# Performance work log

Hardware: AMD Instinct MI355X
Metric: run time of the kernel (lower is better)

Reference implementation:

```python
import jax, jax.numpy as jnp
import numpy as np

C = 768
H = 12
HD = C // H
SCALE = HD ** -0.5
EPS = 1e-5


def setup_inputs() -> dict:
    key = jax.random.key(0)
    kit = iter(jax.random.split(key, 40))
    r = lambda *s: jax.random.normal(next(kit), s, jnp.float32) * 0.02
    d = dict(
        s_x=jax.random.normal(next(kit), (8, 196, C), jnp.float32),
        t_x=jax.random.normal(next(kit), (8, 1568, C), jnp.float32),
        ln1s_g=jnp.ones(C), ln1s_b=jnp.zeros(C),
        mha_w=r(3 * C, C), mha_b=r(3 * C), mha_ow=r(C, C), mha_ob=r(C),
        ln1t_g=jnp.ones(C), ln1t_b=jnp.zeros(C),
        attn_qkv_w=r(3 * C, C), attn_q_b=r(C), attn_v_b=r(C), attn_pw=r(C, C), attn_pb=r(C),
        lnt2s_g=jnp.ones(C), lnt2s_b=jnp.zeros(C),
        t2s_qw=r(C, C), t2s_qb=r(C), t2s_kvw=r(2 * C, C), t2s_kvb=r(C), t2s_pw=r(C, C), t2s_pb=r(C),
        lns2t_g=jnp.ones(C), lns2t_b=jnp.zeros(C),
        s2t_qw=r(C, C), s2t_qb=r(C), s2t_kvw=r(2 * C, C), s2t_kvb=r(C), s2t_pw=r(C, C), s2t_pb=r(C),
        ln2s_g=jnp.ones(C), ln2s_b=jnp.zeros(C),
        cfc_w=r(4 * C, C), cfc_b=r(4 * C), cproj_w=r(C, 4 * C), cproj_b=r(C),
        ln2t_g=jnp.ones(C), ln2t_b=jnp.zeros(C),
        fc1_w=r(4 * C, C), fc1_b=r(4 * C), fc2_w=r(C, 4 * C), fc2_b=r(C),
    )
    return d


def ln(x, g, b):
    m = x.mean(-1, keepdims=True)
    v = jnp.mean((x - m) ** 2, -1, keepdims=True)
    return (x - m) * jax.lax.rsqrt(v + EPS) * g + b


def heads(x):  # (B, N, C) -> (B, H, N, HD)
    B, N, _ = x.shape
    return x.reshape(B, N, H, HD).transpose(0, 2, 1, 3)


def mhsa(q, k, v):  # (B, H, Nq, HD), (B, H, Nk, HD) -> (B, Nq, C)
    a = jax.nn.softmax(jnp.einsum('bhqd,bhkd->bhqk', q * SCALE, k), axis=-1)
    o = jnp.einsum('bhqk,bhkd->bhqd', a, v)
    B, _, Nq, _ = o.shape
    return o.transpose(0, 2, 1, 3).reshape(B, Nq, C)


def reference(s_x, t_x, ln1s_g, ln1s_b, mha_w, mha_b, mha_ow, mha_ob,
              ln1t_g, ln1t_b, attn_qkv_w, attn_q_b, attn_v_b, attn_pw, attn_pb,
              lnt2s_g, lnt2s_b, t2s_qw, t2s_qb, t2s_kvw, t2s_kvb, t2s_pw, t2s_pb,
              lns2t_g, lns2t_b, s2t_qw, s2t_qb, s2t_kvw, s2t_kvb, s2t_pw, s2t_pb,
              ln2s_g, ln2s_b, cfc_w, cfc_b, cproj_w, cproj_b,
              ln2t_g, ln2t_b, fc1_w, fc1_b, fc2_w, fc2_b):
    # 1) clip self-attention. torch nn.MultiheadAttention (batch_first=False)
    # treats axis 0 of the (B, s_N, C) input as the sequence dim, so we
    # faithfully attend over the batch axis.
    y = ln(s_x, ln1s_g, ln1s_b)
    qkv = y @ mha_w.T + mha_b  # (B, s_N, 3C)
    q, k, v = jnp.split(qkv, 3, axis=-1)
    qt, kt, vt = (a.transpose(1, 0, 2) for a in (q, k, v))  # (s_N, B, C)
    o = mhsa(heads(qt), heads(kt), heads(vt))  # (s_N, B, C)
    o = o @ mha_ow.T + mha_ob
    s_x = s_x + o.transpose(1, 0, 2)

    # 2) video-stream self-attention (qkv_bias=True -> cat(q_b, 0, v_b))
    y = ln(t_x, ln1t_g, ln1t_b)
    qkv_bias = jnp.concatenate([attn_q_b, jnp.zeros_like(attn_v_b), attn_v_b])
    qkv = y @ attn_qkv_w.T + qkv_bias
    q, k, v = jnp.split(qkv, 3, axis=-1)
    o = mhsa(heads(q), heads(k), heads(v))
    t_x = t_x + (o @ attn_pw.T + attn_pb)

    # 3) T2S cross: query from LN(s_x), key/value from (updated, un-normed) t_x
    ys = ln(s_x, lnt2s_g, lnt2s_b)
    q = ys @ t2s_qw.T + t2s_qb
    kv = t_x @ t2s_kvw.T + jnp.concatenate([jnp.zeros_like(t2s_kvb), t2s_kvb])
    k, v = jnp.split(kv, 2, axis=-1)
    o = mhsa(heads(q), heads(k), heads(v))
    s_x = s_x + (o @ t2s_pw.T + t2s_pb)

    # 4) S2T cross: query from LN(t_x), key/value from updated s_x
    yt = ln(t_x, lns2t_g, lns2t_b)
    q = yt @ s2t_qw.T + s2t_qb
    kv = s_x @ s2t_kvw.T + jnp.concatenate([jnp.zeros_like(s2t_kvb), s2t_kvb])
    k, v = jnp.split(kv, 2, axis=-1)
    o = mhsa(heads(q), heads(k), heads(v))
    t_x = t_x + (o @ s2t_pw.T + s2t_pb)

    # 5) clip MLP (QuickGELU)
    y = ln(s_x, ln2s_g, ln2s_b)
    h = y @ cfc_w.T + cfc_b
    h = h * jax.nn.sigmoid(1.702 * h)
    s_x = s_x + (h @ cproj_w.T + cproj_b)

    # 6) video MLP (exact GELU, torch default)
    y = ln(t_x, ln2t_g, ln2t_b)
    h = jax.nn.gelu(y @ fc1_w.T + fc1_b, approximate=False)
    t_x = t_x + (h @ fc2_w.T + fc2_b)
    return (s_x, t_x)
```

## Files before the change

kernel.cpp:

```cpp
#include <hip/hip_runtime.h>
#include <stdint.h>


typedef uint16_t u16;
typedef uint16_t u16x8 __attribute__((ext_vector_type(8)));
typedef uint16_t u16x4 __attribute__((ext_vector_type(4)));
typedef short bf16x8 __attribute__((ext_vector_type(8)));
typedef float f32x4 __attribute__((ext_vector_type(4)));

__device__ __forceinline__ float b2f(u16 u) {
    union { float f; uint32_t i; } x;
    x.i = ((uint32_t)u) << 16;
    return x.f;
}
__device__ __forceinline__ u16 f2b(float f) {
    union { float f; uint32_t i; } x;
    x.f = f;
    uint32_t i = x.i;
    uint32_t r = (i + 0x7FFFu + ((i >> 16) & 1u)) >> 16;
    return (u16)r;
}
__device__ __forceinline__ u16 f2b_trunc(float f) {
    union { float f; uint32_t i; } x;
    x.f = f;
    return (u16)(x.i >> 16);
}

__device__ __forceinline__ void gload16(const u16* g, u16* l) {
    __builtin_amdgcn_global_load_lds(
        (const __attribute__((address_space(1))) uint32_t*)g,
        (__attribute__((address_space(3))) uint32_t*)l, 16, 0, 0);
}

__global__ void f2b_kernel(const float* __restrict__ in, u16* __restrict__ out, int n) {
    int i = blockIdx.x * 256 + threadIdx.x;
    if (i < n) out[i] = f2b(in[i]);
}
__global__ void copy_f32(const float* __restrict__ in, float* __restrict__ out, int n) {
    int i = blockIdx.x * 256 + threadIdx.x;
    if (i < n) out[i] = in[i];
}

__global__ void build_bias_pool(float* __restrict__ dst,
    const float* mha_b, const float* attn_q_b, const float* attn_v_b,
    const float* mha_ob, const float* attn_pb, const float* t2s_kvb,
    const float* t2s_qb, const float* t2s_pb, const float* s2t_qb,
    const float* s2t_kvb, const float* s2t_pb, const float* cfc_b,
    const float* cproj_b, const float* fc1_b, const float* fc2_b) {
    int i = blockIdx.x * 256 + threadIdx.x;
    float v = 0.f;
    if (i < 2304) v = mha_b[i];
    else if (i < 4608) { int j = i - 2304; v = (j < 768) ? attn_q_b[j] : (j < 1536 ? 0.f : attn_v_b[j - 1536]); }
    else if (i < 5376) v = mha_ob[i - 4608];
    else if (i < 6144) v = attn_pb[i - 5376];
    else if (i < 7680) { int j = i - 6144; v = (j < 768) ? 0.f : t2s_kvb[j - 768]; }
    else if (i < 8448) v = t2s_qb[i - 7680];
    else if (i < 9216) v = t2s_pb[i - 8448];
    else if (i < 9984) v = s2t_qb[i - 9216];
    else if (i < 11520) { int j = i - 9984; v = (j < 768) ? 0.f : s2t_kvb[j - 768]; }
    else if (i < 12288) v = s2t_pb[i - 11520];
    else if (i < 15360) v = cfc_b[i - 12288];
    else if (i < 16128) v = cproj_b[i - 15360];
    else if (i < 19200) v = fc1_b[i - 16128];
    else if (i < 19968) v = fc2_b[i - 19200];
    else return;
    dst[i] = v;
}

__device__ __forceinline__ float block_sum(float v, float* red) {
    #pragma unroll
    for (int o = 32; o > 0; o >>= 1) v += __shfl_down(v, o, 64);
    int w = threadIdx.x >> 6, l = threadIdx.x & 63;
    __syncthreads();
    if (l == 0) red[w] = v;
    __syncthreads();
    return red[0] + red[1] + red[2] + red[3];
}

__global__ __launch_bounds__(256) void ln_kernel(
    const float* __restrict__ x, const float* __restrict__ g,
    const float* __restrict__ bta, u16* __restrict__ y) {
    const int r = blockIdx.x;
    const int t = threadIdx.x;
    const float* xr = x + (size_t)r * 768;
    float v0 = xr[t], v1 = xr[t + 256], v2 = xr[t + 512];
    __shared__ float red[4];
    float mean = block_sum(v0 + v1 + v2, red) * (1.0f / 768.0f);
    float d0 = v0 - mean, d1 = v1 - mean, d2 = v2 - mean;
    float var = block_sum(d0 * d0 + d1 * d1 + d2 * d2, red) * (1.0f / 768.0f);
    float rs = rsqrtf(var + 1e-5f);
    u16* yr = y + (size_t)r * 768;
    yr[t]       = f2b(d0 * rs * g[t]       + bta[t]);
    yr[t + 256] = f2b(d1 * rs * g[t + 256] + bta[t + 256]);
    yr[t + 512] = f2b(d2 * rs * g[t + 512] + bta[t + 512]);
}

__global__ __launch_bounds__(256) void transpose_v(
    const u16* __restrict__ vp, u16* __restrict__ vt, int Nk, int Nkp,
    long long vA, long long vJ) {
    const int inst = blockIdx.y;
    const int a = inst / 12, h = inst % 12;
    const int t0 = blockIdx.x * 64;
    const int tid = threadIdx.x;
    __shared__ u16 T[64][72];
    const int kvl = tid >> 2, dseg = (tid & 3) * 16;
    u16x8 v0 = {}, v1 = {};
    if (t0 + kvl < Nk) {
        const u16* src = vp + a * vA + (long long)(t0 + kvl) * vJ + h * 64 + dseg;
        v0 = *(const u16x8*)src;
        v1 = *(const u16x8*)(src + 8);
    }
    *(u16x8*)&T[kvl][dseg]     = v0;
    *(u16x8*)&T[kvl][dseg + 8] = v1;
    __syncthreads();
    const int dl = tid >> 2, kseg = (tid & 3) * 16;
    u16x8 w0, w1;
    #pragma unroll
    for (int j = 0; j < 8; j++) w0[j] = T[kseg + j][dl];
    #pragma unroll
    for (int j = 0; j < 8; j++) w1[j] = T[kseg + 8 + j][dl];
    u16* orow = vt + ((size_t)inst * 64 + dl) * Nkp + t0 + kseg;
    *(u16x8*)orow = w0;
    *(u16x8*)(orow + 8) = w1;
}

template <int MODE, int BM>
__global__ __launch_bounds__(256) void gemm_mfma(
    const u16* __restrict__ A, const u16* __restrict__ W,
    const float* __restrict__ bias, u16* __restrict__ Cb,
    float* __restrict__ Cf, int M, int N, int K) {
    constexpr int MI = BM / 32;
    __shared__ u16 As[2][BM][32];
    __shared__ u16 Bs[2][128][32];
    const int tid = threadIdx.x;
    const int lane = tid & 63;
    const int wid = tid >> 6;
    const int wr = (wid >> 1) * (BM / 2), wc = (wid & 1) * 64;
    const int m0 = blockIdx.x * BM, n0 = blockIdx.y * 128;
    const int lr = lane >> 2, lc = (lane & 3) * 8;
    const int fr = lane & 15, fk = (lane >> 4) * 8;
    const int abase = wid * (BM / 4);
    const int bbase = wid * 32;
    f32x4 acc[MI][4] = {};
    for (int k0 = 0; k0 < K; k0 += 64) {
        #pragma unroll
        for (int s = 0; s < 2; s++) {
            #pragma unroll
            for (int j = 0; j < BM / 64; j++) {
                int rowa = m0 + abase + j * 16 + lr;
                rowa = rowa < M ? rowa : M - 1;
                gload16(A + (size_t)rowa * K + k0 + s * 32 + lc, &As[s][abase + j * 16][0]);
            }
            #pragma unroll
            for (int j = 0; j < 2; j++) {
                gload16(W + (size_t)(n0 + bbase + j * 16 + lr) * K + k0 + s * 32 + lc,
                        &Bs[s][bbase + j * 16][0]);
            }
        }
        __syncthreads();
        #pragma unroll
        for (int s = 0; s < 2; s++) {
            bf16x8 a[MI], b[4];
            #pragma unroll
            for (int i = 0; i < MI; i++) a[i] = *(const bf16x8*)&As[s][wr + i * 16 + fr][fk];
            #pragma unroll
            for (int j = 0; j < 4; j++) b[j] = *(const bf16x8*)&Bs[s][wc + j * 16 + fr][fk];
            #pragma unroll
            for (int i = 0; i < MI; i++)
                #pragma unroll
                for (int j = 0; j < 4; j++)
                    acc[i][j] = __builtin_amdgcn_mfma_f32_16x16x32_bf16(a[i], b[j], acc[i][j], 0, 0, 0);
        }
        __syncthreads();
    }
    const int er = (lane >> 4) * 4;
    #pragma unroll
    for (int i = 0; i < MI; i++) {
        #pragma unroll
        for (int reg = 0; reg < 4; reg++) {
            int r = m0 + wr + i * 16 + er + reg;
            if (r >= M) continue;
            #pragma unroll
            for (int j = 0; j < 4; j++) {
                int c = n0 + wc + j * 16 + fr;
                float v = acc[i][j][reg] + bias[c];
                size_t idx = (size_t)r * N + c;
                if (MODE == 1) {
                    Cf[idx] += v;
                } else if (MODE == 4) {
                    float nv = Cf[idx] + v;
                    Cf[idx] = nv;
                    Cb[idx] = f2b(nv);
                } else {
                    if (MODE == 2) v = v / (1.0f + expf(-1.702f * v));
                    if (MODE == 3) v = 0.5f * v * (1.0f + erff(v * 0.70710678118654752f));
                    Cb[idx] = f2b(v);
                }
            }
        }
    }
}

__global__ __launch_bounds__(256) void flash_attn(
    const u16* __restrict__ qp, const u16* __restrict__ kp,
    const u16* __restrict__ vt, u16* __restrict__ op,
    int Nq, int Nk, int Nkp,
    long long qA, long long qI, long long kA, long long kJ,
    long long oA, long long oI) {
    const int inst = blockIdx.y;
    const int a = inst / 12, h = inst % 12;
    const int tid = threadIdx.x, lane = tid & 63, w = tid >> 6;
    const int fr = lane & 15, g = lane >> 4, fk = g * 8;
    const int f3s = (fr & 7) << 3;
    __shared__ u16 Ks[64][64];
    __shared__ u16 Vs[64][64];
    __shared__ u16 Ps[4][16][64];
    const u16* qb = qp + a * qA + h * 64;
    const u16* kb = kp + a * kA + h * 64;
    const u16* vtb = vt + (size_t)inst * 64 * Nkp;
    const int q0 = blockIdx.x * 64 + w * 16;

    bf16x8 qf[2];
    {
        u16x8 raw0 = {}, raw1 = {};
        int qr = q0 + fr;
        if (qr < Nq) {
            const u16* qrp = qb + (long long)qr * qI;
            raw0 = *(const u16x8*)(qrp + fk);
            raw1 = *(const u16x8*)(qrp + 32 + fk);
        }
        const float QS = 0.125f * 1.44269504088896340736f;
        u16x8 s0, s1;
        #pragma unroll
        for (int e = 0; e < 8; e++) {
            s0[e] = f2b(b2f(raw0[e]) * QS);
            s1[e] = f2b(b2f(raw1[e]) * QS);
        }
        qf[0] = *(bf16x8*)&s0;
        qf[1] = *(bf16x8*)&s1;
    }
    float mrun = -1e30f, lrun = 0.f;
    f32x4 o[4] = {};

    const int l = lane;
    const int srow = w * 8 + (l >> 3);
    const int sdcol = ((l & 7) * 8) ^ (((l >> 3) & 7) << 3);

    for (int t0 = 0; t0 < Nk; t0 += 64) {
        #pragma unroll
        for (int c = 0; c < 2; c++) {
            int row = c * 32 + srow;
            int kr = t0 + row; if (kr >= Nk) kr = Nk - 1;
            gload16(kb + (long long)kr * kJ + sdcol, &Ks[0][0] + c * 2048 + w * 512);
            gload16(vtb + (size_t)row * Nkp + t0 + sdcol, &Vs[0][0] + c * 2048 + w * 512);
        }
        __syncthreads();

        f32x4 s[4] = {};
        #pragma unroll
        for (int hh = 0; hh < 4; hh++) {
            bf16x8 k0f = *(const bf16x8*)&Ks[hh * 16 + fr][fk ^ f3s];
            bf16x8 k1f = *(const bf16x8*)&Ks[hh * 16 + fr][(32 + fk) ^ f3s];
            s[hh] = __builtin_amdgcn_mfma_f32_16x16x32_bf16(k0f, qf[0], s[hh], 0, 0, 0);
            s[hh] = __builtin_amdgcn_mfma_f32_16x16x32_bf16(k1f, qf[1], s[hh], 0, 0, 0);
        }
        float lmax = -1e30f;
        if (t0 + 64 <= Nk) {
            #pragma unroll
            for (int hh = 0; hh < 4; hh++)
                #pragma unroll
                for (int r = 0; r < 4; r++) lmax = fmaxf(lmax, s[hh][r]);
        } else {
            #pragma unroll
            for (int hh = 0; hh < 4; hh++)
                #pragma unroll
                for (int r = 0; r < 4; r++) {
                    if (t0 + hh * 16 + 4 * g + r >= Nk) s[hh][r] = -1e30f;
                    lmax = fmaxf(lmax, s[hh][r]);
                }
        }
        lmax = fmaxf(lmax, __shfl_xor(lmax, 16, 64));
        lmax = fmaxf(lmax, __shfl_xor(lmax, 32, 64));
        if (!__all(lmax <= mrun + 8.0f)) {
            float mn = fmaxf(mrun, lmax);
            float sf = exp2f(mrun - mn);
            mrun = mn;
            lrun *= sf;
            float sfo[4];
            #pragma unroll
            for (int r = 0; r < 4; r++) sfo[r] = __shfl(sf, g * 4 + r, 64);
            #pragma unroll
            for (int dt = 0; dt < 4; dt++)
                #pragma unroll
                for (int r = 0; r < 4; r++) o[dt][r] *= sfo[r];
        }
        float p[4][4];
        float ps = 0.f;
        #pragma unroll
        for (int hh = 0; hh < 4; hh++)
            #pragma unroll
            for (int r = 0; r < 4; r++) {
                p[hh][r] = exp2f(s[hh][r] - mrun);
                ps += p[hh][r];
            }
        ps += __shfl_xor(ps, 16, 64);
        ps += __shfl_xor(ps, 32, 64);
        lrun += ps;
        #pragma unroll
        for (int hh = 0; hh < 4; hh++) {
            u16x4 pk;
            #pragma unroll
            for (int r = 0; r < 4; r++) pk[r] = f2b_trunc(p[hh][r]);
            *(u16x4*)&Ps[w][fr][(hh * 16 + g * 4) ^ f3s] = pk;
        }
        bf16x8 pa0 = *(const bf16x8*)&Ps[w][fr][fk ^ f3s];
        bf16x8 pa1 = *(const bf16x8*)&Ps[w][fr][(32 + fk) ^ f3s];
        #pragma unroll
        for (int dt = 0; dt < 4; dt++) {
            bf16x8 vf0 = *(const bf16x8*)&Vs[dt * 16 + fr][fk ^ f3s];
            bf16x8 vf1 = *(const bf16x8*)&Vs[dt * 16 + fr][(32 + fk) ^ f3s];
            o[dt] = __builtin_amdgcn_mfma_f32_16x16x32_bf16(pa0, vf0, o[dt], 0, 0, 0);
            o[dt] = __builtin_amdgcn_mfma_f32_16x16x32_bf16(pa1, vf1, o[dt], 0, 0, 0);
        }
        __syncthreads();
    }
    float rcp = 1.0f / lrun;
    #pragma unroll
    for (int r = 0; r < 4; r++) {
        float rr = __shfl(rcp, g * 4 + r, 64);
        int q = q0 + g * 4 + r;
        if (q >= Nq) continue;
        u16* orow = op + a * oA + (long long)q * oI + h * 64;
        #pragma unroll
        for (int dt = 0; dt < 4; dt++)
            orow[dt * 16 + fr] = f2b(o[dt][r] * rr);
    }
}

extern "C" void kernel_launch(void* const* d_in, const int* in_sizes, int n_in,
                              void* d_out, int out_size, void* d_ws, size_t ws_size,
                              hipStream_t stream) {
    const int B = 8, sN = 196, tN = 1568;
    const int Ms = B * sN;
    const int Mt = B * tN;
    const int n_sf = Ms * 768;
    const int n_tf = Mt * 768;
    (void)n_in; (void)out_size; (void)ws_size;

    const bool dict_order = (in_sizes[0] == n_sf);
    auto IN = [&](int di, int ai) -> const float* {
        return (const float*)d_in[dict_order ? di : ai];
    };
    const float* in_sx      = IN(0, 35);
    const float* in_tx      = IN(1, 42);
    const float* ln1s_g     = IN(2, 14);
    const float* ln1s_b     = IN(3, 13);
    const float* mha_w      = IN(4, 28);
    const float* mha_b      = IN(5, 25);
    const float* mha_ow     = IN(6, 27);
    const float* mha_ob     = IN(7, 26);
    const float* ln1t_g     = IN(8, 16);
    const float* ln1t_b     = IN(9, 15);
    const float* attn_qkv_w = IN(10, 3);
    const float* attn_q_b   = IN(11, 2);
    const float* attn_v_b   = IN(12, 4);
    const float* attn_pw    = IN(13, 1);
    const float* attn_pb    = IN(14, 0);
    const float* lnt2s_g    = IN(15, 24);
    const float* lnt2s_b    = IN(16, 23);
    const float* t2s_qw     = IN(17, 41);
    const float* t2s_qb     = IN(18, 40);
    const float* t2s_kvw    = IN(19, 37);
    const float* t2s_kvb    = IN(20, 36);
    const float* t2s_pw     = IN(21, 39);
    const float* t2s_pb     = IN(22, 38);
    const float* lns2t_g    = IN(23, 22);
    const float* lns2t_b    = IN(24, 21);
    const float* s2t_qw     = IN(25, 34);
    const float* s2t_qb     = IN(26, 33);
    const float* s2t_kvw    = IN(27, 30);
    const float* s2t_kvb    = IN(28, 29);
    const float* s2t_pw     = IN(29, 32);
    const float* s2t_pb     = IN(30, 31);
    const float* ln2s_g     = IN(31, 18);
    const float* ln2s_b     = IN(32, 17);
    const float* cfc_w      = IN(33, 6);
    const float* cfc_b      = IN(34, 5);
    const float* cproj_w    = IN(35, 8);
    const float* cproj_b    = IN(36, 7);
    const float* ln2t_g     = IN(37, 20);
    const float* ln2t_b     = IN(38, 19);
    const float* fc1_w      = IN(39, 10);
    const float* fc1_b      = IN(40, 9);
    const float* fc2_w      = IN(41, 12);
    const float* fc2_b      = IN(42, 11);

    float* s_f = (float*)d_out;
    float* t_f = (float*)d_out + n_sf;

    char* ws = (char*)d_ws;
    size_t off = 0;
    auto take = [&](size_t bytes) { size_t o = off; off += (bytes + 255) & ~(size_t)255; return o; };
    float* biasP = (float*)(ws + take(19968 * 4));
    u16*   yb    = (u16*)(ws + take((size_t)Mt * 768 * 2));
    u16*   bufA  = (u16*)(ws + take((size_t)Mt * 2304 * 2));
    u16*   bufB  = (u16*)(ws + take((size_t)Mt * 768 * 2));
    u16*   sxb   = (u16*)(ws + take((size_t)Ms * 768 * 2));
    u16*   vtb   = (u16*)(ws + take((size_t)2352 * 64 * 64 * 2));
    auto wtake = [&](size_t nelem) { return (u16*)(ws + take(nelem * 2)); };
    u16 *W_mha   = wtake(2304 * 768), *W_mhao  = wtake(768 * 768);
    u16 *W_qkv   = wtake(2304 * 768), *W_attnp = wtake(768 * 768);
    u16 *W_t2sq  = wtake(768 * 768),  *W_t2skv = wtake(1536 * 768), *W_t2sp = wtake(768 * 768);
    u16 *W_s2tq  = wtake(768 * 768),  *W_s2tkv = wtake(1536 * 768), *W_s2tp = wtake(768 * 768);
    u16 *W_cfc   = wtake(3072 * 768), *W_cproj = wtake(768 * 3072);
    u16 *W_fc1   = wtake(3072 * 768), *W_fc2   = wtake(768 * 3072);

    const int B_MHA = 0, B_QKV = 2304, B_MHAO = 4608, B_ATTNP = 5376;
    const int B_T2SKV = 6144, B_T2SQ = 7680, B_T2SP = 8448, B_S2TQ = 9216;
    const int B_S2TKV = 9984, B_S2TP = 11520, B_CFC = 12288, B_CPROJ = 15360;
    const int B_FC1 = 16128, B_FC2 = 19200;

    auto cdiv = [](int a, int b) { return (a + b - 1) / b; };
    auto CW = [&](const float* src, u16* dst, int n) {
        f2b_kernel<<<cdiv(n, 256), 256, 0, stream>>>(src, dst, n);
    };
    CW(mha_w, W_mha, 2304 * 768);      CW(mha_ow, W_mhao, 768 * 768);
    CW(attn_qkv_w, W_qkv, 2304 * 768); CW(attn_pw, W_attnp, 768 * 768);
    CW(t2s_qw, W_t2sq, 768 * 768);     CW(t2s_kvw, W_t2skv, 1536 * 768);
    CW(t2s_pw, W_t2sp, 768 * 768);     CW(s2t_qw, W_s2tq, 768 * 768);
    CW(s2t_kvw, W_s2tkv, 1536 * 768);  CW(s2t_pw, W_s2tp, 768 * 768);
    CW(cfc_w, W_cfc, 3072 * 768);      CW(cproj_w, W_cproj, 768 * 3072);
    CW(fc1_w, W_fc1, 3072 * 768);      CW(fc2_w, W_fc2, 768 * 3072);

    build_bias_pool<<<78, 256, 0, stream>>>(biasP,
        mha_b, attn_q_b, attn_v_b, mha_ob, attn_pb, t2s_kvb, t2s_qb, t2s_pb,
        s2t_qb, s2t_kvb, s2t_pb, cfc_b, cproj_b, fc1_b, fc2_b);

    copy_f32<<<cdiv(n_sf, 256), 256, 0, stream>>>(in_sx, s_f, n_sf);
    copy_f32<<<cdiv(n_tf, 256), 256, 0, stream>>>(in_tx, t_f, n_tf);

    ln_kernel<<<Ms, 256, 0, stream>>>(s_f, ln1s_g, ln1s_b, yb);
    gemm_mfma<0, 64><<<dim3(cdiv(Ms, 64), 18), 256, 0, stream>>>(yb, W_mha, biasP + B_MHA, bufA, (float*)0, Ms, 2304, 768);
    transpose_v<<<dim3(1, sN * 12), 256, 0, stream>>>(bufA + 1536, vtb, 8, 64, 2304LL, (long long)sN * 2304);
    flash_attn<<<dim3(1, sN * 12), 256, 0, stream>>>(
        bufA, bufA + 768, vtb, bufB, 8, 8, 64,
        2304LL, (long long)sN * 2304,
        2304LL, (long long)sN * 2304,
        768LL,  (long long)sN * 768);
    gemm_mfma<1, 64><<<dim3(cdiv(Ms, 64), 6), 256, 0, stream>>>(bufB, W_mhao, biasP + B_MHAO, (u16*)0, s_f, Ms, 768, 768);

    ln_kernel<<<Mt, 256, 0, stream>>>(t_f, ln1t_g, ln1t_b, yb);
    gemm_mfma<0, 128><<<dim3(cdiv(Mt, 128), 18), 256, 0, stream>>>(yb, W_qkv, biasP + B_QKV, bufA, (float*)0, Mt, 2304, 768);
    transpose_v<<<dim3(25, B * 12), 256, 0, stream>>>(bufA + 1536, vtb, tN, 1600, (long long)tN * 2304, 2304LL);
    flash_attn<<<dim3(cdiv(tN, 64), B * 12), 256, 0, stream>>>(
        bufA, bufA + 768, vtb, bufB, tN, tN, 1600,
        (long long)tN * 2304, 2304LL,
        (long long)tN * 2304, 2304LL,
        (long long)tN * 768, 768LL);
    gemm_mfma<4, 128><<<dim3(cdiv(Mt, 128), 6), 256, 0, stream>>>(bufB, W_attnp, biasP + B_ATTNP, yb, t_f, Mt, 768, 768);

    gemm_mfma<0, 128><<<dim3(cdiv(Mt, 128), 12), 256, 0, stream>>>(yb, W_t2skv, biasP + B_T2SKV, bufA, (float*)0, Mt, 1536, 768);
    transpose_v<<<dim3(25, B * 12), 256, 0, stream>>>(bufA + 768, vtb, tN, 1600, (long long)tN * 1536, 1536LL);
    ln_kernel<<<Ms, 256, 0, stream>>>(s_f, lnt2s_g, lnt2s_b, yb);
    u16* q3 = bufB;
    u16* o3 = bufB + (size_t)Ms * 768;
    gemm_mfma<0, 64><<<dim3(cdiv(Ms, 64), 6), 256, 0, stream>>>(yb, W_t2sq, biasP + B_T2SQ, q3, (float*)0, Ms, 768, 768);
    flash_attn<<<dim3(cdiv(sN, 64), B * 12), 256, 0, stream>>>(
        q3, bufA, vtb, o3, sN, tN, 1600,
        (long long)sN * 768, 768LL,
        (long long)tN * 1536, 1536LL,
        (long long)sN * 768, 768LL);
    gemm_mfma<4, 64><<<dim3(cdiv(Ms, 64), 6), 256, 0, stream>>>(o3, W_t2sp, biasP + B_T2SP, sxb, s_f, Ms, 768, 768);

    ln_kernel<<<Mt, 256, 0, stream>>>(t_f, lns2t_g, lns2t_b, yb);
    gemm_mfma<0, 128><<<dim3(cdiv(Mt, 128), 6), 256, 0, stream>>>(yb, W_s2tq, biasP + B_S2TQ, bufB, (float*)0, Mt, 768, 768);
    gemm_mfma<0, 64><<<dim3(cdiv(Ms, 64), 12), 256, 0, stream>>>(sxb, W_s2tkv, biasP + B_S2TKV, bufA, (float*)0, Ms, 1536, 768);
    transpose_v<<<dim3(4, B * 12), 256, 0, stream>>>(bufA + 768, vtb, sN, 256, (long long)sN * 1536, 1536LL);
    flash_attn<<<dim3(cdiv(tN, 64), B * 12), 256, 0, stream>>>(
        bufB, bufA, vtb, yb, tN, sN, 256,
        (long long)tN * 768, 768LL,
        (long long)sN * 1536, 1536LL,
        (long long)tN * 768, 768LL);
    gemm_mfma<1, 128><<<dim3(cdiv(Mt, 128), 6), 256, 0, stream>>>(yb, W_s2tp, biasP + B_S2TP, (u16*)0, t_f, Mt, 768, 768);

    ln_kernel<<<Ms, 256, 0, stream>>>(s_f, ln2s_g, ln2s_b, yb);
    gemm_mfma<2, 64><<<dim3(cdiv(Ms, 64), 24), 256, 0, stream>>>(yb, W_cfc, biasP + B_CFC, bufA, (float*)0, Ms, 3072, 768);
    gemm_mfma<1, 64><<<dim3(cdiv(Ms, 64), 6), 256, 0, stream>>>(bufA, W_cproj, biasP + B_CPROJ, (u16*)0, s_f, Ms, 768, 3072);

    ln_kernel<<<Mt, 256, 0, stream>>>(t_f, ln2t_g, ln2t_b, yb);
    for (int c = 0; c < 2; c++) {
        int r0 = c * (Mt / 2), Mc = Mt / 2;
        gemm_mfma<3, 128><<<dim3(cdiv(Mc, 128), 24), 256, 0, stream>>>(
            yb + (size_t)r0 * 768, W_fc1, biasP + B_FC1, bufA, (float*)0, Mc, 3072, 768);
        gemm_mfma<1, 128><<<dim3(cdiv(Mc, 128), 6), 256, 0, stream>>>(
            bufA, W_fc2, biasP + B_FC2, (u16*)0, t_f + (size_t)r0 * 768, Mc, 768, 3072);
    }
}
```

Measured before the change: 1.089 ms.

## Double-buffer flash attention K/V tiles and merge chunked video MLP GEMMs

```diff
diff --git a/kernel.cpp b/kernel.cpp
--- a/kernel.cpp
+++ b/kernel.cpp
@@ -212,8 +212,8 @@
     const int tid = threadIdx.x, lane = tid & 63, w = tid >> 6;
     const int fr = lane & 15, g = lane >> 4, fk = g * 8;
     const int f3s = (fr & 7) << 3;
-    __shared__ u16 Ks[64][64];
-    __shared__ u16 Vs[64][64];
+    __shared__ u16 Ks[2][64][64];
+    __shared__ u16 Vs[2][64][64];
     __shared__ u16 Ps[4][16][64];
     const u16* qb = qp + a * qA + h * 64;
     const u16* kb = kp + a * kA + h * 64;
@@ -246,39 +246,55 @@
     const int srow = w * 8 + (l >> 3);
     const int sdcol = ((l & 7) * 8) ^ (((l >> 3) & 7) << 3);
 
-    for (int t0 = 0; t0 < Nk; t0 += 64) {
+    auto STAGE = [&](int s, int t0) {
         #pragma unroll
         for (int c = 0; c < 2; c++) {
             int row = c * 32 + srow;
             int kr = t0 + row; if (kr >= Nk) kr = Nk - 1;
-            gload16(kb + (long long)kr * kJ + sdcol, &Ks[0][0] + c * 2048 + w * 512);
-            gload16(vtb + (size_t)row * Nkp + t0 + sdcol, &Vs[0][0] + c * 2048 + w * 512);
-        }
-        __syncthreads();
+            gload16(kb + (long long)kr * kJ + sdcol, &Ks[s][0][0] + c * 2048 + w * 512);
+            gload16(vtb + (size_t)row * Nkp + t0 + sdcol, &Vs[s][0][0] + c * 2048 + w * 512);
+        }
+    };
+
+    const int nt = (Nk + 63) >> 6;
+    STAGE(0, 0);
+    for (int it = 0; it < nt; ++it) {
+        const int t0 = it << 6;
+        const int cur = it & 1;
+        if (it + 1 < nt) {
+            STAGE(cur ^ 1, t0 + 64);
+            asm volatile("s_waitcnt vmcnt(4)" ::: "memory");
+        } else {
+            asm volatile("s_waitcnt vmcnt(0)" ::: "memory");
+        }
+        __builtin_amdgcn_s_barrier();
 
         f32x4 s[4] = {};
+        __builtin_amdgcn_s_setprio(1);
         #pragma unroll
         for (int hh = 0; hh < 4; hh++) {
-            bf16x8 k0f = *(const bf16x8*)&Ks[hh * 16 + fr][fk ^ f3s];
-            bf16x8 k1f = *(const bf16x8*)&Ks[hh * 16 + fr][(32 + fk) ^ f3s];
+            bf16x8 k0f = *(const bf16x8*)&Ks[cur][hh * 16 + fr][fk ^ f3s];
+            bf16x8 k1f = *(const bf16x8*)&Ks[cur][hh * 16 + fr][(32 + fk) ^ f3s];
             s[hh] = __builtin_amdgcn_mfma_f32_16x16x32_bf16(k0f, qf[0], s[hh], 0, 0, 0);
             s[hh] = __builtin_amdgcn_mfma_f32_16x16x32_bf16(k1f, qf[1], s[hh], 0, 0, 0);
         }
-        float lmax = -1e30f;
-        if (t0 + 64 <= Nk) {
+        __builtin_amdgcn_s_setprio(0);
+
+        if (t0 + 64 > Nk) {
             #pragma unroll
             for (int hh = 0; hh < 4; hh++)
                 #pragma unroll
-                for (int r = 0; r < 4; r++) lmax = fmaxf(lmax, s[hh][r]);
-        } else {
-            #pragma unroll
-            for (int hh = 0; hh < 4; hh++)
-                #pragma unroll
-                for (int r = 0; r < 4; r++) {
+                for (int r = 0; r < 4; r++)
                     if (t0 + hh * 16 + 4 * g + r >= Nk) s[hh][r] = -1e30f;
-                    lmax = fmaxf(lmax, s[hh][r]);
-                }
-        }
+        }
+        float a0 = fmaxf(fmaxf(s[0][0], s[0][1]), s[0][2]);
+        float a1 = fmaxf(fmaxf(s[0][3], s[1][0]), s[1][1]);
+        float a2 = fmaxf(fmaxf(s[1][2], s[1][3]), s[2][0]);
+        float a3 = fmaxf(fmaxf(s[2][1], s[2][2]), s[2][3]);
+        float a4 = fmaxf(fmaxf(s[3][0], s[3][1]), s[3][2]);
+        float b0 = fmaxf(fmaxf(a0, a1), a2);
+        float b1 = fmaxf(fmaxf(a3, a4), s[3][3]);
+        float lmax = fmaxf(b0, b1);
         lmax = fmaxf(lmax, __shfl_xor(lmax, 16, 64));
         lmax = fmaxf(lmax, __shfl_xor(lmax, 32, 64));
         if (!__all(lmax <= mrun + 8.0f)) {
@@ -315,14 +331,16 @@
         }
         bf16x8 pa0 = *(const bf16x8*)&Ps[w][fr][fk ^ f3s];
         bf16x8 pa1 = *(const bf16x8*)&Ps[w][fr][(32 + fk) ^ f3s];
+        __builtin_amdgcn_s_setprio(1);
         #pragma unroll
         for (int dt = 0; dt < 4; dt++) {
-            bf16x8 vf0 = *(const bf16x8*)&Vs[dt * 16 + fr][fk ^ f3s];
-            bf16x8 vf1 = *(const bf16x8*)&Vs[dt * 16 + fr][(32 + fk) ^ f3s];
+            bf16x8 vf0 = *(const bf16x8*)&Vs[cur][dt * 16 + fr][fk ^ f3s];
+            bf16x8 vf1 = *(const bf16x8*)&Vs[cur][dt * 16 + fr][(32 + fk) ^ f3s];
             o[dt] = __builtin_amdgcn_mfma_f32_16x16x32_bf16(pa0, vf0, o[dt], 0, 0, 0);
             o[dt] = __builtin_amdgcn_mfma_f32_16x16x32_bf16(pa1, vf1, o[dt], 0, 0, 0);
         }
-        __syncthreads();
+        __builtin_amdgcn_s_setprio(0);
+        __builtin_amdgcn_s_barrier();
     }
     float rcp = 1.0f / lrun;
     #pragma unroll
@@ -403,7 +421,7 @@
     auto take = [&](size_t bytes) { size_t o = off; off += (bytes + 255) & ~(size_t)255; return o; };
     float* biasP = (float*)(ws + take(19968 * 4));
     u16*   yb    = (u16*)(ws + take((size_t)Mt * 768 * 2));
-    u16*   bufA  = (u16*)(ws + take((size_t)Mt * 2304 * 2));
+    u16*   bufA  = (u16*)(ws + take((size_t)Mt * 3072 * 2));
     u16*   bufB  = (u16*)(ws + take((size_t)Mt * 768 * 2));
     u16*   sxb   = (u16*)(ws + take((size_t)Ms * 768 * 2));
     u16*   vtb   = (u16*)(ws + take((size_t)2352 * 64 * 64 * 2));
@@ -488,11 +506,6 @@
     gemm_mfma<1, 64><<<dim3(cdiv(Ms, 64), 6), 256, 0, stream>>>(bufA, W_cproj, biasP + B_CPROJ, (u16*)0, s_f, Ms, 768, 3072);
 
     ln_kernel<<<Mt, 256, 0, stream>>>(t_f, ln2t_g, ln2t_b, yb);
-    for (int c = 0; c < 2; c++) {
-        int r0 = c * (Mt / 2), Mc = Mt / 2;
-        gemm_mfma<3, 128><<<dim3(cdiv(Mc, 128), 24), 256, 0, stream>>>(
-            yb + (size_t)r0 * 768, W_fc1, biasP + B_FC1, bufA, (float*)0, Mc, 3072, 768);
-        gemm_mfma<1, 128><<<dim3(cdiv(Mc, 128), 6), 256, 0, stream>>>(
-            bufA, W_fc2, biasP + B_FC2, (u16*)0, t_f + (size_t)r0 * 768, Mc, 768, 3072);
-    }
-}
+    gemm_mfma<3, 128><<<dim3(cdiv(Mt, 128), 24), 256, 0, stream>>>(yb, W_fc1, biasP + B_FC1, bufA, (float*)0, Mt, 3072, 768);
+    gemm_mfma<1, 128><<<dim3(cdiv(Mt, 128), 6), 256, 0, stream>>>(bufA, W_fc2, biasP + B_FC2, (u16*)0, t_f, Mt, 768, 3072);
+}
```

Result: faster. 1.050 ms (-3.6%).
